# Kernel tuning notes

Measured on AMD Instinct MI355X. Metric: run time of the kernel, lower is better.

The kernel has to match this reference:

```python
import jax, jax.numpy as jnp
import numpy as np

VOCAB = 4823          # round(feature_size_criteo[512])
EMB = 128             # embedding_size
B = 16384             # batch
N_SPARSE = 26
N_DENSE = 13
HID = 256


def setup_inputs() -> dict:
    key = jax.random.key(0)
    ks = jax.random.split(key, 8)
    dense_input = jax.random.normal(ks[0], (B, N_DENSE), dtype=jnp.float32)
    sparse_input = jax.random.randint(ks[1], (B, N_SPARSE), 0, VOCAB, dtype=jnp.int32)
    emb1 = jax.random.normal(ks[2], (VOCAB, 1), dtype=jnp.float32) * 0.02
    emb2 = jax.random.normal(ks[3], (VOCAB, EMB), dtype=jnp.float32) * 0.02
    fm_w = jax.random.normal(ks[4], (1, N_DENSE), dtype=jnp.float32) * 0.1
    w1 = jax.random.normal(ks[5], (HID, N_SPARSE * EMB), dtype=jnp.float32) * (1.0 / np.sqrt(N_SPARSE * EMB))
    w2 = jax.random.normal(ks[6], (HID, HID), dtype=jnp.float32) * (1.0 / np.sqrt(HID))
    w3 = jax.random.normal(ks[7], (1, HID), dtype=jnp.float32) * (1.0 / np.sqrt(HID))
    return {"dense_input": dense_input, "sparse_input": sparse_input,
            "emb1": emb1, "emb2": emb2, "fm_w": fm_w,
            "w1": w1, "w2": w2, "w3": w3}


def reference(dense_input, sparse_input, emb1, emb2, fm_w, w1, w2, w3):
    # first-order FM part
    sparse_1dim = emb1[sparse_input]                     # [B, 26, 1]
    fm_dense = dense_input @ fm_w.T                      # [B, 1]
    fm_sparse = jnp.sum(sparse_1dim, axis=1)             # [B, 1]
    y1 = fm_dense + fm_sparse

    # second-order FM part (sum-square minus square-sum trick)
    sparse_2dim = emb2[sparse_input]                     # [B, 26, EMB]
    s = jnp.sum(sparse_2dim, axis=1)                     # [B, EMB]
    ss = jnp.sum(jnp.square(sparse_2dim), axis=1)        # [B, EMB]
    y2 = 0.5 * jnp.sum(jnp.square(s) - ss, axis=1, keepdims=True)  # [B, 1]

    # deep MLP part
    flat = sparse_2dim.reshape(-1, N_SPARSE * EMB)       # [B, 26*EMB]
    h = jax.nn.relu(flat @ w1.T)
    h = jax.nn.relu(h @ w2.T)
    y3 = h @ w3.T                                        # [B, 1]

    return jax.nn.sigmoid(y1 + y2 + y3)
```

## Files before the change

### kernel.cpp

```cpp
#include <hip/hip_runtime.h>
#include <cstdint>
#include <cstddef>


#define B_ROWS   16384
#define NSPARSE  26
#define NDENSE   13
#define EMBD     128
#define HID      256
#define K1       (NSPARSE*EMBD)
#define VOCAB    4823
#define PAD_V    4864
#define NP       (NSPARSE*HID)

typedef unsigned short ushort_t;
typedef __attribute__((ext_vector_type(8))) short bf16x8;
typedef __attribute__((ext_vector_type(8))) unsigned short ushort8;
typedef __attribute__((ext_vector_type(4))) float f32x4;

__device__ __forceinline__ ushort_t f32_bf16(float x) {
    unsigned u = __builtin_bit_cast(unsigned, x);
    u += 0x7fffu + ((u >> 16) & 1u);
    return (ushort_t)(u >> 16);
}
__device__ __forceinline__ float bf16_f32(ushort_t h) {
    return __builtin_bit_cast(float, ((unsigned)h) << 16);
}

__device__ __forceinline__ void gl2lds16(const void* g, void* l) {
    __builtin_amdgcn_global_load_lds(
        (const __attribute__((address_space(1))) void*)g,
        (__attribute__((address_space(3))) void*)l, 16, 0, 0);
}

__global__ __launch_bounds__(256) void prep_kernel(
    const float* __restrict__ emb2, const float* __restrict__ w1,
    const float* __restrict__ w2, ushort_t* __restrict__ e2b,
    ushort_t* __restrict__ b1b, ushort_t* __restrict__ w2b) {
    constexpr int NA = VOCAB * EMBD / 4;
    constexpr int NB = NP * EMBD / 4;
    constexpr int NC = HID * HID / 4;
    int i = blockIdx.x * 256 + threadIdx.x;
    float4 x;
    ushort_t* dst;
    int di;
    if (i < NA) {
        x = ((const float4*)emb2)[i]; dst = e2b; di = i;
    } else if (i < NA + NB) {
        int j = i - NA;
        int c = j & 31, rowp = j >> 5;
        int f = rowp >> 8, h = rowp & 255;
        x = ((const float4*)w1)[h * (K1 / 4) + f * 32 + c];
        dst = b1b; di = j;
    } else if (i < NA + NB + NC) {
        int j = i - NA - NB;
        x = ((const float4*)w2)[j]; dst = w2b; di = j;
    } else return;
    union { ushort_t u[4]; uint2 v; } H;
    float xs[4] = {x.x, x.y, x.z, x.w};
#pragma unroll
    for (int j = 0; j < 4; ++j) H.u[j] = f32_bf16(xs[j]);
    ((uint2*)dst)[di] = H.v;
}

__global__ __launch_bounds__(256) void gemm_p_kernel(
    const ushort_t* __restrict__ A, const ushort_t* __restrict__ Bm,
    ushort_t* __restrict__ P2) {
    __shared__ union {
        struct { ushort_t a[128 * 128]; ushort_t b[128 * 128]; } s;
        ushort_t t[128 * 128];
    } sm;
    const int tid = threadIdx.x;
    const int bm = blockIdx.x, bn = blockIdx.y;
    const int lane = tid & 63, wv = tid >> 6;

#pragma unroll
    for (int i = 0; i < 8; ++i) {
        int s = (wv * 8 + i) * 64 + lane;
        int row = s >> 4, g = s & 15;
        int gs = g ^ (row & 7);
        gl2lds16(A  + (size_t)(bm * 128 + row) * EMBD + gs * 8, &sm.s.a[s * 8]);
        gl2lds16(Bm + (size_t)(bn * 128 + row) * EMBD + gs * 8, &sm.s.b[s * 8]);
    }
    __syncthreads();

    const int wr = wv >> 1, wc = wv & 1;
    const int lrow = lane & 15, lq = lane >> 4;
    f32x4 acc[4][4] = {};
#pragma unroll
    for (int ks = 0; ks < 4; ++ks) {
        bf16x8 af[4], bf[4];
#pragma unroll
        for (int m = 0; m < 4; ++m) {
            int row = wr * 64 + m * 16 + lrow;
            int g = (ks * 4 + lq) ^ (row & 7);
            af[m] = *(const bf16x8*)&sm.s.a[row * 128 + g * 8];
        }
#pragma unroll
        for (int n = 0; n < 4; ++n) {
            int row = wc * 64 + n * 16 + lrow;
            int g = (ks * 4 + lq) ^ (row & 7);
            bf[n] = *(const bf16x8*)&sm.s.b[row * 128 + g * 8];
        }
#pragma unroll
        for (int m = 0; m < 4; ++m)
#pragma unroll
            for (int n = 0; n < 4; ++n)
                acc[m][n] = __builtin_amdgcn_mfma_f32_16x16x32_bf16(af[m], bf[n], acc[m][n], 0, 0, 0);
    }
    __syncthreads();

#pragma unroll
    for (int m = 0; m < 4; ++m)
#pragma unroll
        for (int n = 0; n < 4; ++n) {
            int col = wc * 64 + n * 16 + lrow;
#pragma unroll
            for (int r = 0; r < 4; ++r) {
                int row = wr * 64 + m * 16 + lq * 4 + r;
                sm.t[row * 128 + col] = f32_bf16(acc[m][n][r]);
            }
        }
    __syncthreads();
    const int f0 = bn >> 1, half = bn & 1;
    const int r0 = tid >> 4, c16 = tid & 15;
#pragma unroll
    for (int k = 0; k < 8; ++k) {
        int row = r0 + k * 16;
        ushort8 v8 = *(const ushort8*)&sm.t[row * 128 + c16 * 8];
        *(ushort8*)&P2[((size_t)f0 * PAD_V + bm * 128 + row) * HID + half * 128 + c16 * 8] = v8;
    }
}

#define H1LD 264
__global__ __launch_bounds__(256) void mega_kernel(
    const ushort_t* __restrict__ P2, const ushort_t* __restrict__ e2b,
    const ushort_t* __restrict__ w2b, const float* __restrict__ dense,
    const int* __restrict__ sidx, const float* __restrict__ emb1,
    const float* __restrict__ fm_w, const float* __restrict__ w3,
    float* __restrict__ out) {
    __shared__ int      sI[16 * NSPARSE];
    __shared__ ushort_t h1s[16 * H1LD];
    __shared__ float    y12s[16];
    __shared__ float    y3s[4][16];

    const int tid = threadIdx.x;
    const int b0 = blockIdx.x * 16;
    for (int i = tid; i < 16 * NSPARSE; i += 256) sI[i] = sidx[b0 * NSPARSE + i];
    __syncthreads();

    const int row = tid >> 4, h16 = tid & 15;
    float hacc[16] = {};
    float s8[8] = {};
    float ss = 0.f;
#pragma unroll 4
    for (int f = 0; f < NSPARSE; ++f) {
        int v = sI[row * NSPARSE + f];
        const ushort_t* pp = P2 + ((size_t)f * PAD_V + v) * HID + h16 * 16;
        ushort8 p0 = *(const ushort8*)pp;
        ushort8 p1 = *(const ushort8*)(pp + 8);
        ushort8 ev = *(const ushort8*)(e2b + (size_t)v * EMBD + h16 * 8);
#pragma unroll
        for (int j = 0; j < 8; ++j) {
            hacc[j]     += bf16_f32(p0[j]);
            hacc[8 + j] += bf16_f32(p1[j]);
            float e = bf16_f32(ev[j]);
            s8[j] += e; ss += e * e;
        }
    }
    {
        union { ushort_t u[8]; ushort8 v; } o0, o1;
#pragma unroll
        for (int j = 0; j < 8; ++j) {
            o0.u[j] = f32_bf16(fmaxf(hacc[j], 0.f));
            o1.u[j] = f32_bf16(fmaxf(hacc[8 + j], 0.f));
        }
        *(ushort8*)&h1s[row * H1LD + h16 * 16]     = o0.v;
        *(ushort8*)&h1s[row * H1LD + h16 * 16 + 8] = o1.v;
    }
    float part = 0.f;
#pragma unroll
    for (int j = 0; j < 8; ++j) part += s8[j] * s8[j];
    part = 0.5f * (part - ss);
    if (h16 < NDENSE) {
        part += dense[(b0 + row) * NDENSE + h16] * fm_w[h16];
        part += emb1[sI[row * NSPARSE + h16]] + emb1[sI[row * NSPARSE + 13 + h16]];
    }
#pragma unroll
    for (int o = 8; o; o >>= 1) part += __shfl_xor(part, o, 64);
    if (h16 == 0) y12s[row] = part;
    __syncthreads();

    const int lane = tid & 63, wv = tid >> 6;
    const int lrow = lane & 15, lq = lane >> 4;
    f32x4 acc[4] = {};
#pragma unroll
    for (int ks = 0; ks < 8; ++ks) {
        bf16x8 af = *(const bf16x8*)&h1s[lrow * H1LD + ks * 32 + lq * 8];
#pragma unroll
        for (int nt = 0; nt < 4; ++nt) {
            bf16x8 bf = *(const bf16x8*)&w2b[(size_t)(wv * 64 + nt * 16 + lrow) * HID + ks * 32 + lq * 8];
            acc[nt] = __builtin_amdgcn_mfma_f32_16x16x32_bf16(af, bf, acc[nt], 0, 0, 0);
        }
    }
    float y3p[4] = {};
#pragma unroll
    for (int nt = 0; nt < 4; ++nt) {
        float wv3 = w3[wv * 64 + nt * 16 + lrow];
#pragma unroll
        for (int r = 0; r < 4; ++r) y3p[r] += fmaxf(acc[nt][r], 0.f) * wv3;
    }
#pragma unroll
    for (int r = 0; r < 4; ++r)
#pragma unroll
        for (int o = 8; o; o >>= 1) y3p[r] += __shfl_xor(y3p[r], o, 64);
    if (lrow == 0)
#pragma unroll
        for (int r = 0; r < 4; ++r) y3s[wv][lq * 4 + r] = y3p[r];
    __syncthreads();
    if (tid < 16) {
        float z = y12s[tid] + y3s[0][tid] + y3s[1][tid] + y3s[2][tid] + y3s[3][tid];
        out[b0 + tid] = 1.f / (1.f + __expf(-z));
    }
}

extern "C" void kernel_launch(void* const* d_in, const int* in_sizes, int n_in,
                              void* d_out, int out_size, void* d_ws, size_t ws_size,
                              hipStream_t stream) {
    const float* dense = (const float*)d_in[0];
    const int*   sidx  = (const int*)d_in[1];
    const float* emb1  = (const float*)d_in[2];
    const float* emb2  = (const float*)d_in[3];
    const float* fm_w  = (const float*)d_in[4];
    const float* w1    = (const float*)d_in[5];
    const float* w2    = (const float*)d_in[6];
    const float* w3    = (const float*)d_in[7];
    float* out = (float*)d_out;

    char* p = (char*)d_ws;
    auto carve = [&](size_t bytes) { void* r = (void*)p; p += (bytes + 255) & ~(size_t)255; return r; };
    ushort_t* e2b = (ushort_t*)carve((size_t)PAD_V * EMBD * 2);
    ushort_t* b1b = (ushort_t*)carve((size_t)NP * EMBD * 2);
    ushort_t* w2b = (ushort_t*)carve((size_t)HID * HID * 2);
    ushort_t* P2  = (ushort_t*)carve((size_t)NSPARSE * PAD_V * HID * 2);

    constexpr int NPREP = (VOCAB * EMBD + NP * EMBD + HID * HID) / 4;
    prep_kernel<<<(NPREP + 255) / 256, 256, 0, stream>>>(emb2, w1, w2, e2b, b1b, w2b);

    gemm_p_kernel<<<dim3(PAD_V / 128, NP / 128), 256, 0, stream>>>(e2b, b1b, P2);

    mega_kernel<<<B_ROWS / 16, 256, 0, stream>>>(
        P2, e2b, w2b, dense, sidx, emb1, fm_w, w3, out);
}
```

Measured before the change: 139.1 us.

## Store precomputed per-feature projection table in scaled FP8 instead of BF16

The precomputed table of embedding-times-W1 projections is now quantized to FP8 with a power-of-two scale folded into W1, and the scale is undone through w3. This halves the bytes written by the table GEMM and gathered per sample in the main kernel, where the gather is the dominant traffic. The gather loop is split from the embedding-sum loop, fully unrolled, and the kernel gets an occupancy hint. FP8 quantization of the summed projections adds numeric error that could break the tolerance check.

```diff
diff --git a/kernel.cpp b/kernel.cpp
--- a/kernel.cpp
+++ b/kernel.cpp
@@ -12,11 +12,15 @@
 #define VOCAB    4823
 #define PAD_V    4864
 #define NP       (NSPARSE*HID)
+#define PSCALE   128.0f
+#define PINV     (1.0f/128.0f)
 
 typedef unsigned short ushort_t;
+typedef unsigned char  uchar_t;
 typedef __attribute__((ext_vector_type(8))) short bf16x8;
 typedef __attribute__((ext_vector_type(8))) unsigned short ushort8;
 typedef __attribute__((ext_vector_type(4))) float f32x4;
+typedef __attribute__((ext_vector_type(2))) float f32x2;
 
 __device__ __forceinline__ ushort_t f32_bf16(float x) {
     unsigned u = __builtin_bit_cast(unsigned, x);
@@ -25,6 +29,14 @@
 }
 __device__ __forceinline__ float bf16_f32(ushort_t h) {
     return __builtin_bit_cast(float, ((unsigned)h) << 16);
+}
+__device__ __forceinline__ void dec8acc(int a, int b, float* h) {
+    f32x2 r0 = __builtin_amdgcn_cvt_pk_f32_fp8(a, false);
+    f32x2 r1 = __builtin_amdgcn_cvt_pk_f32_fp8(a, true);
+    f32x2 r2 = __builtin_amdgcn_cvt_pk_f32_fp8(b, false);
+    f32x2 r3 = __builtin_amdgcn_cvt_pk_f32_fp8(b, true);
+    h[0] += r0.x; h[1] += r0.y; h[2] += r1.x; h[3] += r1.y;
+    h[4] += r2.x; h[5] += r2.y; h[6] += r3.x; h[7] += r3.y;
 }
 
 __device__ __forceinline__ void gl2lds16(const void* g, void* l) {
@@ -44,6 +56,7 @@
     float4 x;
     ushort_t* dst;
     int di;
+    float sc = 1.f;
     if (i < NA) {
         x = ((const float4*)emb2)[i]; dst = e2b; di = i;
     } else if (i < NA + NB) {
@@ -51,7 +64,7 @@
         int c = j & 31, rowp = j >> 5;
         int f = rowp >> 8, h = rowp & 255;
         x = ((const float4*)w1)[h * (K1 / 4) + f * 32 + c];
-        dst = b1b; di = j;
+        dst = b1b; di = j; sc = PSCALE;
     } else if (i < NA + NB + NC) {
         int j = i - NA - NB;
         x = ((const float4*)w2)[j]; dst = w2b; di = j;
@@ -59,16 +72,16 @@
     union { ushort_t u[4]; uint2 v; } H;
     float xs[4] = {x.x, x.y, x.z, x.w};
 #pragma unroll
-    for (int j = 0; j < 4; ++j) H.u[j] = f32_bf16(xs[j]);
+    for (int j = 0; j < 4; ++j) H.u[j] = f32_bf16(xs[j] * sc);
     ((uint2*)dst)[di] = H.v;
 }
 
 __global__ __launch_bounds__(256) void gemm_p_kernel(
     const ushort_t* __restrict__ A, const ushort_t* __restrict__ Bm,
-    ushort_t* __restrict__ P2) {
+    uchar_t* __restrict__ P2) {
     __shared__ union {
         struct { ushort_t a[128 * 128]; ushort_t b[128 * 128]; } s;
-        ushort_t t[128 * 128];
+        uchar_t t[128 * 128];
     } sm;
     const int tid = threadIdx.x;
     const int bm = blockIdx.x, bn = blockIdx.y;
@@ -118,23 +131,25 @@
 #pragma unroll
             for (int r = 0; r < 4; ++r) {
                 int row = wr * 64 + m * 16 + lq * 4 + r;
-                sm.t[row * 128 + col] = f32_bf16(acc[m][n][r]);
+                float v = acc[m][n][r];
+                int e = __builtin_amdgcn_cvt_pk_fp8_f32(v, v, 0, false);
+                sm.t[row * 128 + col] = (uchar_t)(e & 0xff);
             }
         }
     __syncthreads();
     const int f0 = bn >> 1, half = bn & 1;
-    const int r0 = tid >> 4, c16 = tid & 15;
-#pragma unroll
-    for (int k = 0; k < 8; ++k) {
-        int row = r0 + k * 16;
-        ushort8 v8 = *(const ushort8*)&sm.t[row * 128 + c16 * 8];
-        *(ushort8*)&P2[((size_t)f0 * PAD_V + bm * 128 + row) * HID + half * 128 + c16 * 8] = v8;
+    const int r8 = tid >> 3, c8 = tid & 7;
+#pragma unroll
+    for (int k = 0; k < 4; ++k) {
+        int row = k * 32 + r8;
+        int4 v16 = *(const int4*)&sm.t[row * 128 + c8 * 16];
+        *(int4*)&P2[((size_t)f0 * PAD_V + bm * 128 + row) * HID + half * 128 + c8 * 16] = v16;
     }
 }
 
 #define H1LD 264
-__global__ __launch_bounds__(256) void mega_kernel(
-    const ushort_t* __restrict__ P2, const ushort_t* __restrict__ e2b,
+__global__ __launch_bounds__(256, 4) void mega_kernel(
+    const uchar_t* __restrict__ P2, const ushort_t* __restrict__ e2b,
     const ushort_t* __restrict__ w2b, const float* __restrict__ dense,
     const int* __restrict__ sidx, const float* __restrict__ emb1,
     const float* __restrict__ fm_w, const float* __restrict__ w3,
@@ -150,20 +165,24 @@
     __syncthreads();
 
     const int row = tid >> 4, h16 = tid & 15;
+    const int* rI = sI + row * NSPARSE;
+
     float hacc[16] = {};
+#pragma unroll
+    for (int f = 0; f < NSPARSE; ++f) {
+        int v = rI[f];
+        int4 q = *(const int4*)(P2 + ((size_t)f * PAD_V + v) * HID + h16 * 16);
+        dec8acc(q.x, q.y, &hacc[0]);
+        dec8acc(q.z, q.w, &hacc[8]);
+    }
     float s8[8] = {};
     float ss = 0.f;
-#pragma unroll 4
+#pragma unroll
     for (int f = 0; f < NSPARSE; ++f) {
-        int v = sI[row * NSPARSE + f];
-        const ushort_t* pp = P2 + ((size_t)f * PAD_V + v) * HID + h16 * 16;
-        ushort8 p0 = *(const ushort8*)pp;
-        ushort8 p1 = *(const ushort8*)(pp + 8);
+        int v = rI[f];
         ushort8 ev = *(const ushort8*)(e2b + (size_t)v * EMBD + h16 * 8);
 #pragma unroll
         for (int j = 0; j < 8; ++j) {
-            hacc[j]     += bf16_f32(p0[j]);
-            hacc[8 + j] += bf16_f32(p1[j]);
             float e = bf16_f32(ev[j]);
             s8[j] += e; ss += e * e;
         }
@@ -184,7 +203,7 @@
     part = 0.5f * (part - ss);
     if (h16 < NDENSE) {
         part += dense[(b0 + row) * NDENSE + h16] * fm_w[h16];
-        part += emb1[sI[row * NSPARSE + h16]] + emb1[sI[row * NSPARSE + 13 + h16]];
+        part += emb1[rI[h16]] + emb1[rI[13 + h16]];
     }
 #pragma unroll
     for (int o = 8; o; o >>= 1) part += __shfl_xor(part, o, 64);
@@ -206,7 +225,7 @@
     float y3p[4] = {};
 #pragma unroll
     for (int nt = 0; nt < 4; ++nt) {
-        float wv3 = w3[wv * 64 + nt * 16 + lrow];
+        float wv3 = w3[wv * 64 + nt * 16 + lrow] * PINV;
 #pragma unroll
         for (int r = 0; r < 4; ++r) y3p[r] += fmaxf(acc[nt][r], 0.f) * wv3;
     }
@@ -242,7 +261,7 @@
     ushort_t* e2b = (ushort_t*)carve((size_t)PAD_V * EMBD * 2);
     ushort_t* b1b = (ushort_t*)carve((size_t)NP * EMBD * 2);
     ushort_t* w2b = (ushort_t*)carve((size_t)HID * HID * 2);
-    ushort_t* P2  = (ushort_t*)carve((size_t)NSPARSE * PAD_V * HID * 2);
+    uchar_t*  P2  = (uchar_t*)carve((size_t)NSPARSE * PAD_V * HID);
 
     constexpr int NPREP = (VOCAB * EMBD + NP * EMBD + HID * HID) / 4;
     prep_kernel<<<(NPREP + 255) / 256, 256, 0, stream>>>(emb2, w1, w2, e2b, b1b, w2b);
```

Result: slower. 163.5 us (+17.5%).
